# Performance work log

Hardware: AMD Instinct MI355X
Metric: run time of the kernel (lower is better)

The kernel has to match this reference:

```python
import jax, jax.numpy as jnp
import numpy as np

B = 512      # batch
T = 128      # decoder horizon -> T-1 = 127 steps
DNH = 128    # decoder_num_hidden
ENC = 2 * DNH   # encoder_num_hidden (required by attn concat: 3*ENC == 6*DNH)
H = 2 * DNH     # LSTM hidden size


def setup_inputs() -> dict:
    key = jax.random.key(0)
    ks = jax.random.split(key, 10)
    def w(k, shape, scale=0.05):
        return jax.random.normal(k, shape, jnp.float32) * scale
    return {
        "X_encoded": jax.random.normal(ks[0], (B, T - 1, ENC), jnp.float32),
        "y_prev":    jax.random.normal(ks[1], (B, T - 1), jnp.float32),
        # attn_layer: Linear(6*DNH -> DNH) then Linear(DNH -> 1)
        "W_attn1": w(ks[2], (DNH, 6 * DNH)), "b_attn1": jnp.zeros((DNH,), jnp.float32),
        "W_attn2": w(ks[3], (1, DNH)),       "b_attn2": jnp.zeros((1,), jnp.float32),
        # fc: Linear(2*DNH+1 -> 1)
        "W_fc": w(ks[4], (1, 2 * DNH + 1)),  "b_fc": jnp.zeros((1,), jnp.float32),
        # single-layer LSTM, input_size=1, hidden=H, PyTorch gate order (i,f,g,o)
        "W_ih": w(ks[5], (4 * H, 1)), "W_hh": w(ks[6], (4 * H, H)),
        "b_ih": jnp.zeros((4 * H,), jnp.float32), "b_hh": jnp.zeros((4 * H,), jnp.float32),
        # fc_final: Linear(4*DNH -> 1)
        "W_final": w(ks[7], (1, 4 * DNH)), "b_final": jnp.zeros((1,), jnp.float32),
    }


def reference(X_encoded, y_prev, W_attn1, b_attn1, W_attn2, b_attn2,
              W_fc, b_fc, W_ih, W_hh, b_ih, b_hh, W_final, b_final):
    Bz, Tm1, E = X_encoded.shape
    Hh = W_hh.shape[1]
    d0 = jnp.zeros((Bz, Hh), X_encoded.dtype)
    c0 = jnp.zeros((Bz, Hh), X_encoded.dtype)

    def step(carry, y_t):
        d, c = carry                                   # (B, H) each
        state = jnp.concatenate([d, c], axis=-1)[:, None, :]        # (B,1,2H)
        x = jnp.concatenate(
            [jnp.broadcast_to(state, (Bz, Tm1, 2 * Hh)), X_encoded], axis=-1)  # (B,T-1,6*DNH)
        a = x @ W_attn1.T + b_attn1                    # (B,T-1,DNH)
        score = (a @ W_attn2.T + b_attn2)[..., 0]      # (B,T-1)
        beta = jax.nn.softmax(score, axis=1)
        context = jnp.einsum('bt,bte->be', beta, X_encoded)          # (B,E)
        y = jnp.concatenate([context, y_t[:, None]], axis=-1)        # (B,E+1)
        y_tilde = y @ W_fc.T + b_fc                    # (B,1)
        gates = y_tilde @ W_ih.T + b_ih + d @ W_hh.T + b_hh          # (B,4H)
        i, f, g, o = jnp.split(gates, 4, axis=-1)
        i, f, o = jax.nn.sigmoid(i), jax.nn.sigmoid(f), jax.nn.sigmoid(o)
        g = jnp.tanh(g)
        c_new = f * c + i * g
        d_new = o * jnp.tanh(c_new)
        return (d_new, c_new), context

    (dT, _), contexts = jax.lax.scan(step, (d0, c0), y_prev.T)
    y_pred = jnp.concatenate([dT, contexts[-1]], axis=-1) @ W_final.T + b_final  # (B,1)
    return y_pred
```

## Files before the change

kernel.cpp:

```cpp
#include <hip/hip_runtime.h>
#include <stdint.h>

typedef __attribute__((ext_vector_type(8))) short short8;
typedef __attribute__((ext_vector_type(8))) unsigned short ushort8_t;
typedef __attribute__((ext_vector_type(4))) float floatx4;

#define T1 127
#define ENC 256
#define HD 256

#define WHI_OFF   0u
#define WLO_OFF   524288u
#define D0_OFF    1048576u
#define D1_OFF    1572864u
#define WEFF_OFF  2097152u
#define YT_OFF    2099200u
#define CTX_OFF   2361344u
#define DT_OFF    2885632u

__device__ __forceinline__ void split_bf16(float x, unsigned& hi, unsigned& lo) {
    unsigned u = __float_as_uint(x);
    hi = u >> 16;
    float hf = __uint_as_float(hi << 16);
    float r = x - hf;
    unsigned ur = __float_as_uint(r);
    lo = (ur + 0x7fffu + ((ur >> 16) & 1u)) >> 16;
}

__device__ __forceinline__ float sigm_f(float x) { return 1.f / (1.f + __expf(-x)); }
__device__ __forceinline__ float tanh_f(float x) {
    x = fminf(9.f, fmaxf(-9.f, x));
    float e = __expf(2.f * x);
    return (e - 1.f) / (e + 1.f);
}

__global__ __launch_bounds__(256) void k_prep(const float* __restrict__ W1,
                                              const float* __restrict__ W2,
                                              const float* __restrict__ W_hh,
                                              char* __restrict__ ws) {
    const int tid = threadIdx.x, bid = blockIdx.x;
    ushort* Whi = (ushort*)(ws + WHI_OFF);
    ushort* Wlo = (ushort*)(ws + WLO_OFF);
    {
        const int i4 = bid * 256 + tid;
        float4 v = ((const float4*)W_hh)[i4];
        float vv[4] = {v.x, v.y, v.z, v.w};
        unsigned h[4], l[4];
        #pragma unroll
        for (int j = 0; j < 4; ++j) split_bf16(vv[j], h[j], l[j]);
        *(ushort4*)(Whi + i4 * 4) = make_ushort4((ushort)h[0], (ushort)h[1], (ushort)h[2], (ushort)h[3]);
        *(ushort4*)(Wlo + i4 * 4) = make_ushort4((ushort)l[0], (ushort)l[1], (ushort)l[2], (ushort)l[3]);
    }
    {
        const int idx = bid * 256 + tid;
        if (idx < 32768) ((uint4*)(ws + D0_OFF))[idx] = make_uint4(0, 0, 0, 0);
    }
    if (bid == 0) {
        float acc = 0.f;
        for (int j = 0; j < 128; ++j)
            acc = fmaf(W2[j], W1[j * 768 + 512 + tid], acc);
        ((float*)(ws + WEFF_OFF))[tid] = acc;
    }
}

__global__ __launch_bounds__(256) void k_attn(const float* __restrict__ X,
                                              const float* __restrict__ y_prev,
                                              const float* __restrict__ W_fc,
                                              const float* __restrict__ b_fc,
                                              char* __restrict__ ws) {
    __shared__ float s_lds[128];
    __shared__ float beta[128];
    __shared__ float red[256];
    const int b = blockIdx.x, tid = threadIdx.x;
    const int w = tid >> 6, lane = tid & 63;
    const float* Xb = X + (size_t)b * T1 * ENC;
    const float* weff = (const float*)(ws + WEFF_OFF);
    const float4 w4 = ((const float4*)weff)[lane];
    for (int i = 0; i < 32; ++i) {
        int t = w * 32 + i;
        if (t >= T1) break;
        float4 x4 = ((const float4*)(Xb + t * ENC))[lane];
        float a = x4.x * w4.x + x4.y * w4.y + x4.z * w4.z + x4.w * w4.w;
        for (int m = 32; m >= 1; m >>= 1) a += __shfl_xor(a, m, 64);
        if (lane == 0) s_lds[t] = a;
    }
    __syncthreads();
    if (w == 0) {
        float v0 = s_lds[lane];
        float v1 = (lane + 64 < T1) ? s_lds[lane + 64] : -1e30f;
        float mx = fmaxf(v0, v1);
        for (int m = 32; m >= 1; m >>= 1) mx = fmaxf(mx, __shfl_xor(mx, m, 64));
        float e0 = __expf(v0 - mx);
        float e1 = (lane + 64 < T1) ? __expf(v1 - mx) : 0.f;
        float s = e0 + e1;
        for (int m = 32; m >= 1; m >>= 1) s += __shfl_xor(s, m, 64);
        float inv = 1.f / s;
        beta[lane] = e0 * inv;
        if (lane + 64 < T1) beta[lane + 64] = e1 * inv;
    }
    __syncthreads();
    float acc = 0.f;
    for (int t = 0; t < T1; ++t) acc = fmaf(beta[t], Xb[t * ENC + tid], acc);
    ((float*)(ws + CTX_OFF))[b * ENC + tid] = acc;
    red[tid] = acc * W_fc[tid];
    __syncthreads();
    for (int s = 128; s >= 1; s >>= 1) { if (tid < s) red[tid] += red[tid + s]; __syncthreads(); }
    const float u = red[0] + b_fc[0];
    const float wy = W_fc[256];
    if (tid < T1)
        ((float*)(ws + YT_OFF))[b * 128 + tid] = u + wy * y_prev[b * T1 + tid];
}

__global__ __launch_bounds__(256, 1) void k_lstm(const float* __restrict__ W_ih,
                                                 const float* __restrict__ b_ih,
                                                 const float* __restrict__ b_hh,
                                                 char* __restrict__ ws) {
    __shared__ __align__(16) ushort ldh[16 * 264];
    __shared__ __align__(16) ushort ldl[16 * 264];
    __shared__ float gbuf[16 * 132];

    const int tid = threadIdx.x, bid = blockIdx.x;
    const int gi = bid >> 3, hj = bid & 7;
    const int w = tid >> 6, lane = tid & 63;
    const int n16 = lane & 15, q = lane >> 4;

    const ushort* Whi = (const ushort*)(ws + WHI_OFF);
    const ushort* Wlo = (const ushort*)(ws + WLO_OFF);
    unsigned long long* Dbuf0 = (unsigned long long*)(ws + D0_OFF);
    unsigned long long* Dbuf1 = (unsigned long long*)(ws + D1_OFF);
    const float* yt = (const float*)(ws + YT_OFF);
    float* dT = (float*)(ws + DT_OFF);

    short8 bfh[2][8], bfl[2][8];
    #pragma unroll
    for (int j = 0; j < 2; ++j) {
        const int r = (2 * w + j) * 16 + n16;
        const int hloc = r >> 2, g = r & 3;
        const int R = g * 256 + hj * 32 + hloc;
        #pragma unroll
        for (int kt = 0; kt < 8; ++kt) {
            bfh[j][kt] = *(const short8*)(Whi + R * 256 + kt * 32 + q * 8);
            bfl[j][kt] = *(const short8*)(Wlo + R * 256 + kt * 32 + q * 8);
        }
    }

    const int b_loc = tid & 15, hpair = tid >> 4;
    const int hloc0 = hpair * 2;
    const int bg = gi * 16 + b_loc;
    float wihr[2][4], bihr[2][4];
    #pragma unroll
    for (int jj = 0; jj < 2; ++jj)
        #pragma unroll
        for (int g = 0; g < 4; ++g) {
            const int row = g * HD + hj * 32 + hloc0 + jj;
            wihr[jj][g] = W_ih[row];
            bihr[jj][g] = b_ih[row] + b_hh[row];
        }
    float cc0 = 0.f, cc1 = 0.f;

    const int pb = tid >> 4, hp8 = tid & 15;
    const bool own = ((hp8 >> 1) == hj);
    const size_t pbase = (size_t)(gi * 16 + pb) * 128 + hp8 * 8;

    {
        ushort8_t z = {0, 0, 0, 0, 0, 0, 0, 0};
        *(ushort8_t*)(ldh + pb * 264 + hp8 * 16)     = z;
        *(ushort8_t*)(ldh + pb * 264 + hp8 * 16 + 8) = z;
        *(ushort8_t*)(ldl + pb * 264 + hp8 * 16)     = z;
        *(ushort8_t*)(ldl + pb * 264 + hp8 * 16 + 8) = z;
    }

    for (int t = 1; t <= T1; ++t) {
        const float ytv = yt[bg * 128 + (t - 1)];
        if (!own) {
            unsigned long long* Dsrc = ((t - 1) & 1) ? Dbuf1 : Dbuf0;
            const unsigned e = (unsigned)(t - 1) & 3u;
            unsigned long long wv[8];
            #pragma unroll
            for (int i = 0; i < 8; ++i)
                wv[i] = __hip_atomic_load(&Dsrc[pbase + i], __ATOMIC_RELAXED,
                                          __HIP_MEMORY_SCOPE_AGENT);
            unsigned stale = 0xFFu;
            for (;;) {
                unsigned ns = 0;
                #pragma unroll
                for (int i = 0; i < 8; ++i)
                    if (stale & (1u << i)) {
                        unsigned ep = (unsigned)(wv[i] & 1ull) |
                                      (((unsigned)(wv[i] >> 32) & 1u) << 1);
                        if (ep != e) ns |= 1u << i;
                    }
                if (!ns) break;
                __builtin_amdgcn_s_sleep(1);
                #pragma unroll
                for (int i = 0; i < 8; ++i)
                    if (ns & (1u << i))
                        wv[i] = __hip_atomic_load(&Dsrc[pbase + i], __ATOMIC_RELAXED,
                                                  __HIP_MEMORY_SCOPE_AGENT);
                stale = ns;
            }
            ushort hv[16], lv[16];
            #pragma unroll
            for (int i = 0; i < 8; ++i) {
                hv[2 * i]     = (ushort)((wv[i] >> 16) & 0xFFFFull);
                hv[2 * i + 1] = (ushort)(wv[i] >> 48);
                lv[2 * i]     = (ushort)(wv[i] & 0xFFFEull);
                lv[2 * i + 1] = (ushort)((wv[i] >> 32) & 0xFFFEull);
            }
            ushort8_t H0, L0;
            #pragma unroll
            for (int i = 0; i < 8; ++i) { H0[i] = hv[i]; L0[i] = lv[i]; }
            ushort8_t H1, L1;
            #pragma unroll
            for (int i = 0; i < 8; ++i) { H1[i] = hv[8 + i]; L1[i] = lv[8 + i]; }
            *(ushort8_t*)(ldh + pb * 264 + hp8 * 16)     = H0;
            *(ushort8_t*)(ldh + pb * 264 + hp8 * 16 + 8) = H1;
            *(ushort8_t*)(ldl + pb * 264 + hp8 * 16)     = L0;
            *(ushort8_t*)(ldl + pb * 264 + hp8 * 16 + 8) = L1;
        }
        __syncthreads();
        floatx4 acc0 = {0.f, 0.f, 0.f, 0.f}, acc1 = {0.f, 0.f, 0.f, 0.f};
        #pragma unroll
        for (int kt = 0; kt < 8; ++kt) {
            short8 ah = *(const short8*)(ldh + n16 * 264 + kt * 32 + q * 8);
            short8 al = *(const short8*)(ldl + n16 * 264 + kt * 32 + q * 8);
            acc0 = __builtin_amdgcn_mfma_f32_16x16x32_bf16(ah, bfh[0][kt], acc0, 0, 0, 0);
            acc0 = __builtin_amdgcn_mfma_f32_16x16x32_bf16(al, bfh[0][kt], acc0, 0, 0, 0);
            acc0 = __builtin_amdgcn_mfma_f32_16x16x32_bf16(ah, bfl[0][kt], acc0, 0, 0, 0);
            acc1 = __builtin_amdgcn_mfma_f32_16x16x32_bf16(ah, bfh[1][kt], acc1, 0, 0, 0);
            acc1 = __builtin_amdgcn_mfma_f32_16x16x32_bf16(al, bfh[1][kt], acc1, 0, 0, 0);
            acc1 = __builtin_amdgcn_mfma_f32_16x16x32_bf16(ah, bfl[1][kt], acc1, 0, 0, 0);
        }
        #pragma unroll
        for (int reg = 0; reg < 4; ++reg) {
            gbuf[(q * 4 + reg) * 132 + (2 * w) * 16 + n16]     = acc0[reg];
            gbuf[(q * 4 + reg) * 132 + (2 * w + 1) * 16 + n16] = acc1[reg];
        }
        __syncthreads();
        float dnew[2];
        #pragma unroll
        for (int jj = 0; jj < 2; ++jj) {
            const int base = b_loc * 132 + (hloc0 + jj) * 4;
            float pi = gbuf[base + 0] + ytv * wihr[jj][0] + bihr[jj][0];
            float pf = gbuf[base + 1] + ytv * wihr[jj][1] + bihr[jj][1];
            float pg = gbuf[base + 2] + ytv * wihr[jj][2] + bihr[jj][2];
            float po = gbuf[base + 3] + ytv * wihr[jj][3] + bihr[jj][3];
            float ig = sigm_f(pi), fg = sigm_f(pf), og = sigm_f(po);
            float gg = tanh_f(pg);
            float& c = jj ? cc1 : cc0;
            c = fg * c + ig * gg;
            dnew[jj] = og * tanh_f(c);
        }
        if (t < T1) {
            const unsigned e = (unsigned)t & 3u;
            unsigned h0, l0, h1, l1;
            split_bf16(dnew[0], h0, l0);
            split_bf16(dnew[1], h1, l1);
            l0 = (l0 & 0xFFFEu) | (e & 1u);
            l1 = (l1 & 0xFFFEu) | ((e >> 1) & 1u);
            *(ushort2*)(ldh + b_loc * 264 + hj * 32 + hloc0) =
                make_ushort2((ushort)h0, (ushort)h1);
            *(ushort2*)(ldl + b_loc * 264 + hj * 32 + hloc0) =
                make_ushort2((ushort)(l0 & 0xFFFEu), (ushort)(l1 & 0xFFFEu));
            unsigned long long wv = ((unsigned long long)h1 << 48) |
                                    ((unsigned long long)l1 << 32) |
                                    ((unsigned long long)h0 << 16) |
                                    (unsigned long long)l0;
            unsigned long long* Ddst = (t & 1) ? Dbuf1 : Dbuf0;
            __hip_atomic_store(&Ddst[(size_t)bg * 128 + hj * 16 + hpair], wv,
                               __ATOMIC_RELAXED, __HIP_MEMORY_SCOPE_AGENT);
        } else {
            *(float2*)(dT + bg * 256 + hj * 32 + hloc0) = make_float2(dnew[0], dnew[1]);
        }
    }
}

__global__ __launch_bounds__(256) void k_final(const float* __restrict__ W_final,
                                               const float* __restrict__ b_final,
                                               float* __restrict__ out,
                                               char* __restrict__ ws) {
    __shared__ float red[256];
    const int b = blockIdx.x, tid = threadIdx.x;
    const float* dT = (const float*)(ws + DT_OFF);
    const float* ctx = (const float*)(ws + CTX_OFF);
    float v = W_final[tid] * dT[b * 256 + tid] + W_final[256 + tid] * ctx[b * 256 + tid];
    red[tid] = v;
    __syncthreads();
    for (int s = 128; s >= 1; s >>= 1) { if (tid < s) red[tid] += red[tid + s]; __syncthreads(); }
    if (tid == 0) out[b] = red[0] + b_final[0];
}

extern "C" void kernel_launch(void* const* d_in, const int* in_sizes, int n_in,
                              void* d_out, int out_size, void* d_ws, size_t ws_size,
                              hipStream_t stream) {
    const float* X      = (const float*)d_in[0];
    const float* y_prev = (const float*)d_in[1];
    const float* W1     = (const float*)d_in[2];
    const float* W2     = (const float*)d_in[4];
    const float* W_fc   = (const float*)d_in[6];
    const float* b_fc   = (const float*)d_in[7];
    const float* W_ih   = (const float*)d_in[8];
    const float* W_hh   = (const float*)d_in[9];
    const float* b_ih   = (const float*)d_in[10];
    const float* b_hh   = (const float*)d_in[11];
    const float* W_fin  = (const float*)d_in[12];
    const float* b_fin  = (const float*)d_in[13];
    char* ws = (char*)d_ws;

    hipLaunchKernelGGL(k_prep,  dim3(256), dim3(256), 0, stream, W1, W2, W_hh, ws);
    hipLaunchKernelGGL(k_attn,  dim3(512), dim3(256), 0, stream, X, y_prev, W_fc, b_fc, ws);
    hipLaunchKernelGGL(k_lstm,  dim3(256), dim3(256), 0, stream, W_ih, b_ih, b_hh, ws);
    hipLaunchKernelGGL(k_final, dim3(512), dim3(256), 0, stream, W_fin, b_fin, (float*)d_out, ws);
}
```

Measured before the change: 655.2 us.

## Remap LSTM blocks to XCD-local groups and poll with vectorized sc0 loads

Block IDs are remapped so the eight hidden-slice blocks of one batch group land on the same XCD under round-robin dispatch, letting cross-block state exchange stay in a shared L2. The per-step handoff poll is replaced by four wide dwordx4 loads with the sc0 cache bit plus a bounded retry, falling back to the original per-word agent-scope atomic polling if it times out. Each publish now issues a plain non-atomic global store before the existing atomic store. The intent is to cut cross-XCD coherence latency on the serial 127-step chain. The cost is a reliance on the undocumented dispatch-to-XCD mapping and on a weaker cache coherence scope, plus one redundant store per step.

```diff
diff --git a/kernel.cpp b/kernel.cpp
--- a/kernel.cpp
+++ b/kernel.cpp
@@ -32,6 +32,18 @@
     x = fminf(9.f, fmaxf(-9.f, x));
     float e = __expf(2.f * x);
     return (e - 1.f) / (e + 1.f);
+}
+
+__device__ __forceinline__ void load64_sc0(const unsigned long long* p,
+                                           uint4& a, uint4& b, uint4& c, uint4& d) {
+    asm volatile("global_load_dwordx4 %0, %4, off sc0\n\t"
+                 "global_load_dwordx4 %1, %4, off offset:16 sc0\n\t"
+                 "global_load_dwordx4 %2, %4, off offset:32 sc0\n\t"
+                 "global_load_dwordx4 %3, %4, off offset:48 sc0\n\t"
+                 "s_waitcnt vmcnt(0)"
+                 : "=v"(a), "=v"(b), "=v"(c), "=v"(d)
+                 : "v"((unsigned long long)p)
+                 : "memory");
 }
 
 __global__ __launch_bounds__(256) void k_prep(const float* __restrict__ W1,
@@ -120,7 +132,8 @@
     __shared__ float gbuf[16 * 132];
 
     const int tid = threadIdx.x, bid = blockIdx.x;
-    const int gi = bid >> 3, hj = bid & 7;
+    const int gi = (bid & 7) * 4 + (bid >> 6);
+    const int hj = (bid >> 3) & 7;
     const int w = tid >> 6, lane = tid & 63;
     const int n16 = lane & 15, q = lane >> 4;
 
@@ -161,6 +174,7 @@
     const int pb = tid >> 4, hp8 = tid & 15;
     const bool own = ((hp8 >> 1) == hj);
     const size_t pbase = (size_t)(gi * 16 + pb) * 128 + hp8 * 8;
+    bool fast = true;
 
     {
         ushort8_t z = {0, 0, 0, 0, 0, 0, 0, 0};
@@ -175,44 +189,69 @@
         if (!own) {
             unsigned long long* Dsrc = ((t - 1) & 1) ? Dbuf1 : Dbuf0;
             const unsigned e = (unsigned)(t - 1) & 3u;
-            unsigned long long wv[8];
-            #pragma unroll
-            for (int i = 0; i < 8; ++i)
-                wv[i] = __hip_atomic_load(&Dsrc[pbase + i], __ATOMIC_RELAXED,
-                                          __HIP_MEMORY_SCOPE_AGENT);
-            unsigned stale = 0xFFu;
-            for (;;) {
-                unsigned ns = 0;
+            unsigned lo[8], hi[8];
+            bool got = false;
+            if (fast) {
+                for (int rr = 0; rr < 24; ++rr) {
+                    uint4 A, B, C, D;
+                    load64_sc0(&Dsrc[pbase], A, B, C, D);
+                    lo[0] = A.x; hi[0] = A.y; lo[1] = A.z; hi[1] = A.w;
+                    lo[2] = B.x; hi[2] = B.y; lo[3] = B.z; hi[3] = B.w;
+                    lo[4] = C.x; hi[4] = C.y; lo[5] = C.z; hi[5] = C.w;
+                    lo[6] = D.x; hi[6] = D.y; lo[7] = D.z; hi[7] = D.w;
+                    bool ok = true;
+                    #pragma unroll
+                    for (int i = 0; i < 8; ++i) {
+                        unsigned ep = (lo[i] & 1u) | ((hi[i] & 1u) << 1);
+                        ok &= (ep == e);
+                    }
+                    if (ok) { got = true; break; }
+                    __builtin_amdgcn_s_sleep(1);
+                }
+                if (!got) fast = false;
+            }
+            if (!got) {
+                unsigned long long wv[8];
                 #pragma unroll
                 for (int i = 0; i < 8; ++i)
-                    if (stale & (1u << i)) {
-                        unsigned ep = (unsigned)(wv[i] & 1ull) |
-                                      (((unsigned)(wv[i] >> 32) & 1u) << 1);
-                        if (ep != e) ns |= 1u << i;
-                    }
-                if (!ns) break;
-                __builtin_amdgcn_s_sleep(1);
+                    wv[i] = __hip_atomic_load(&Dsrc[pbase + i], __ATOMIC_RELAXED,
+                                              __HIP_MEMORY_SCOPE_AGENT);
+                unsigned stale = 0xFFu;
+                for (;;) {
+                    unsigned ns = 0;
+                    #pragma unroll
+                    for (int i = 0; i < 8; ++i)
+                        if (stale & (1u << i)) {
+                            unsigned ep = (unsigned)(wv[i] & 1ull) |
+                                          (((unsigned)(wv[i] >> 32) & 1u) << 1);
+                            if (ep != e) ns |= 1u << i;
+                        }
+                    if (!ns) break;
+                    __builtin_amdgcn_s_sleep(1);
+                    #pragma unroll
+                    for (int i = 0; i < 8; ++i)
+                        if (ns & (1u << i))
+                            wv[i] = __hip_atomic_load(&Dsrc[pbase + i], __ATOMIC_RELAXED,
+                                                      __HIP_MEMORY_SCOPE_AGENT);
+                    stale = ns;
+                }
                 #pragma unroll
-                for (int i = 0; i < 8; ++i)
-                    if (ns & (1u << i))
-                        wv[i] = __hip_atomic_load(&Dsrc[pbase + i], __ATOMIC_RELAXED,
-                                                  __HIP_MEMORY_SCOPE_AGENT);
-                stale = ns;
+                for (int i = 0; i < 8; ++i) {
+                    lo[i] = (unsigned)wv[i];
+                    hi[i] = (unsigned)(wv[i] >> 32);
+                }
             }
             ushort hv[16], lv[16];
             #pragma unroll
             for (int i = 0; i < 8; ++i) {
-                hv[2 * i]     = (ushort)((wv[i] >> 16) & 0xFFFFull);
-                hv[2 * i + 1] = (ushort)(wv[i] >> 48);
-                lv[2 * i]     = (ushort)(wv[i] & 0xFFFEull);
-                lv[2 * i + 1] = (ushort)((wv[i] >> 32) & 0xFFFEull);
+                hv[2 * i]     = (ushort)(lo[i] >> 16);
+                hv[2 * i + 1] = (ushort)(hi[i] >> 16);
+                lv[2 * i]     = (ushort)(lo[i] & 0xFFFEu);
+                lv[2 * i + 1] = (ushort)(hi[i] & 0xFFFEu);
             }
-            ushort8_t H0, L0;
+            ushort8_t H0, L0, H1, L1;
             #pragma unroll
-            for (int i = 0; i < 8; ++i) { H0[i] = hv[i]; L0[i] = lv[i]; }
-            ushort8_t H1, L1;
-            #pragma unroll
-            for (int i = 0; i < 8; ++i) { H1[i] = hv[8 + i]; L1[i] = lv[8 + i]; }
+            for (int i = 0; i < 8; ++i) { H0[i] = hv[i]; L0[i] = lv[i]; H1[i] = hv[8 + i]; L1[i] = lv[8 + i]; }
             *(ushort8_t*)(ldh + pb * 264 + hp8 * 16)     = H0;
             *(ushort8_t*)(ldh + pb * 264 + hp8 * 16 + 8) = H1;
             *(ushort8_t*)(ldl + pb * 264 + hp8 * 16)     = L0;
@@ -267,8 +306,10 @@
                                     ((unsigned long long)h0 << 16) |
                                     (unsigned long long)l0;
             unsigned long long* Ddst = (t & 1) ? Dbuf1 : Dbuf0;
-            __hip_atomic_store(&Ddst[(size_t)bg * 128 + hj * 16 + hpair], wv,
-                               __ATOMIC_RELAXED, __HIP_MEMORY_SCOPE_AGENT);
+            unsigned long long* dstp = &Ddst[(size_t)bg * 128 + hj * 16 + hpair];
+            asm volatile("global_store_dwordx2 %0, %1, off"
+                         :: "v"((unsigned long long)dstp), "v"(wv) : "memory");
+            __hip_atomic_store(dstp, wv, __ATOMIC_RELAXED, __HIP_MEMORY_SCOPE_AGENT);
         } else {
             *(float2*)(dT + bg * 256 + hj * 32 + hloc0) = make_float2(dnew[0], dnew[1]);
         }
```

Measured after the change: 1.194 ms. 82.2% more time.

## Process two batch groups per LSTM block, interleaving their recurrent steps

Applied to the files above, without the earlier changes.

Each LSTM block now handles two 16-row batch groups instead of one, halving the grid to 128 blocks. Within each timestep it processes the groups one after the other, so one group's cross-block exchange wait can overlap with work on the other, and the register-resident W_hh fragments are reused across both groups. The spin-wait also skips s_sleep for the first two polling rounds to cut wake-up latency. The cost is twice the serial work per block per step and half as many active CUs, so the latency-bound recurrence may lengthen.

```diff
diff --git a/kernel.cpp b/kernel.cpp
--- a/kernel.cpp
+++ b/kernel.cpp
@@ -115,12 +115,12 @@
                                                  const float* __restrict__ b_ih,
                                                  const float* __restrict__ b_hh,
                                                  char* __restrict__ ws) {
-    __shared__ __align__(16) ushort ldh[16 * 264];
-    __shared__ __align__(16) ushort ldl[16 * 264];
+    __shared__ __align__(16) ushort ldh[2][4224];
+    __shared__ __align__(16) ushort ldl[2][4224];
     __shared__ float gbuf[16 * 132];
 
-    const int tid = threadIdx.x, bid = blockIdx.x;
-    const int gi = bid >> 3, hj = bid & 7;
+    const int tid = threadIdx.x, bk = blockIdx.x;
+    const int hj = bk & 7, pi = bk >> 3;
     const int w = tid >> 6, lane = tid & 63;
     const int n16 = lane & 15, q = lane >> 4;
 
@@ -146,7 +146,7 @@
 
     const int b_loc = tid & 15, hpair = tid >> 4;
     const int hloc0 = hpair * 2;
-    const int bg = gi * 16 + b_loc;
+    const int bgs[2] = { (2 * pi) * 16 + b_loc, (2 * pi + 1) * 16 + b_loc };
     float wihr[2][4], bihr[2][4];
     #pragma unroll
     for (int jj = 0; jj < 2; ++jj)
@@ -156,121 +156,129 @@
             wihr[jj][g] = W_ih[row];
             bihr[jj][g] = b_ih[row] + b_hh[row];
         }
-    float cc0 = 0.f, cc1 = 0.f;
+    float cc[2][2] = {{0.f, 0.f}, {0.f, 0.f}};
 
     const int pb = tid >> 4, hp8 = tid & 15;
     const bool own = ((hp8 >> 1) == hj);
-    const size_t pbase = (size_t)(gi * 16 + pb) * 128 + hp8 * 8;
+    const size_t pbases[2] = {
+        ((size_t)((2 * pi) * 16 + pb)) * 128 + hp8 * 8,
+        ((size_t)((2 * pi + 1) * 16 + pb)) * 128 + hp8 * 8
+    };
 
     {
         ushort8_t z = {0, 0, 0, 0, 0, 0, 0, 0};
-        *(ushort8_t*)(ldh + pb * 264 + hp8 * 16)     = z;
-        *(ushort8_t*)(ldh + pb * 264 + hp8 * 16 + 8) = z;
-        *(ushort8_t*)(ldl + pb * 264 + hp8 * 16)     = z;
-        *(ushort8_t*)(ldl + pb * 264 + hp8 * 16 + 8) = z;
+        #pragma unroll
+        for (int s = 0; s < 2; ++s) {
+            *(ushort8_t*)(&ldh[s][pb * 264 + hp8 * 16])     = z;
+            *(ushort8_t*)(&ldh[s][pb * 264 + hp8 * 16 + 8]) = z;
+            *(ushort8_t*)(&ldl[s][pb * 264 + hp8 * 16])     = z;
+            *(ushort8_t*)(&ldl[s][pb * 264 + hp8 * 16 + 8]) = z;
+        }
     }
 
     for (int t = 1; t <= T1; ++t) {
-        const float ytv = yt[bg * 128 + (t - 1)];
-        if (!own) {
-            unsigned long long* Dsrc = ((t - 1) & 1) ? Dbuf1 : Dbuf0;
-            const unsigned e = (unsigned)(t - 1) & 3u;
-            unsigned long long wv[8];
-            #pragma unroll
-            for (int i = 0; i < 8; ++i)
-                wv[i] = __hip_atomic_load(&Dsrc[pbase + i], __ATOMIC_RELAXED,
-                                          __HIP_MEMORY_SCOPE_AGENT);
-            unsigned stale = 0xFFu;
-            for (;;) {
-                unsigned ns = 0;
+        #pragma unroll
+        for (int s = 0; s < 2; ++s) {
+            const int bg = bgs[s];
+            const float ytv = yt[bg * 128 + (t - 1)];
+            if (!own) {
+                unsigned long long* Dsrc = ((t - 1) & 1) ? Dbuf1 : Dbuf0;
+                const unsigned e = (unsigned)(t - 1) & 3u;
+                const size_t pbase = pbases[s];
+                unsigned long long wv[8];
                 #pragma unroll
                 for (int i = 0; i < 8; ++i)
-                    if (stale & (1u << i)) {
-                        unsigned ep = (unsigned)(wv[i] & 1ull) |
-                                      (((unsigned)(wv[i] >> 32) & 1u) << 1);
-                        if (ep != e) ns |= 1u << i;
-                    }
-                if (!ns) break;
-                __builtin_amdgcn_s_sleep(1);
+                    wv[i] = __hip_atomic_load(&Dsrc[pbase + i], __ATOMIC_RELAXED,
+                                              __HIP_MEMORY_SCOPE_AGENT);
+                unsigned stale = 0xFFu;
+                for (int round = 0; ; ++round) {
+                    unsigned ns = 0;
+                    #pragma unroll
+                    for (int i = 0; i < 8; ++i)
+                        if (stale & (1u << i)) {
+                            unsigned ep = (unsigned)(wv[i] & 1ull) |
+                                          (((unsigned)(wv[i] >> 32) & 1u) << 1);
+                            if (ep != e) ns |= 1u << i;
+                        }
+                    if (!ns) break;
+                    if (round >= 2) __builtin_amdgcn_s_sleep(1);
+                    #pragma unroll
+                    for (int i = 0; i < 8; ++i)
+                        if (ns & (1u << i))
+                            wv[i] = __hip_atomic_load(&Dsrc[pbase + i], __ATOMIC_RELAXED,
+                                                      __HIP_MEMORY_SCOPE_AGENT);
+                    stale = ns;
+                }
+                ushort hv[16], lv[16];
                 #pragma unroll
-                for (int i = 0; i < 8; ++i)
-                    if (ns & (1u << i))
-                        wv[i] = __hip_atomic_load(&Dsrc[pbase + i], __ATOMIC_RELAXED,
-                                                  __HIP_MEMORY_SCOPE_AGENT);
-                stale = ns;
-            }
-            ushort hv[16], lv[16];
+                for (int i = 0; i < 8; ++i) {
+                    hv[2 * i]     = (ushort)((wv[i] >> 16) & 0xFFFFull);
+                    hv[2 * i + 1] = (ushort)(wv[i] >> 48);
+                    lv[2 * i]     = (ushort)(wv[i] & 0xFFFEull);
+                    lv[2 * i + 1] = (ushort)((wv[i] >> 32) & 0xFFFEull);
+                }
+                ushort8_t H0, L0, H1, L1;
+                #pragma unroll
+                for (int i = 0; i < 8; ++i) { H0[i] = hv[i]; L0[i] = lv[i]; H1[i] = hv[8 + i]; L1[i] = lv[8 + i]; }
+                *(ushort8_t*)(&ldh[s][pb * 264 + hp8 * 16])     = H0;
+                *(ushort8_t*)(&ldh[s][pb * 264 + hp8 * 16 + 8]) = H1;
+                *(ushort8_t*)(&ldl[s][pb * 264 + hp8 * 16])     = L0;
+                *(ushort8_t*)(&ldl[s][pb * 264 + hp8 * 16 + 8]) = L1;
+            }
+            __syncthreads();
+            floatx4 acc0 = {0.f, 0.f, 0.f, 0.f}, acc1 = {0.f, 0.f, 0.f, 0.f};
             #pragma unroll
-            for (int i = 0; i < 8; ++i) {
-                hv[2 * i]     = (ushort)((wv[i] >> 16) & 0xFFFFull);
-                hv[2 * i + 1] = (ushort)(wv[i] >> 48);
-                lv[2 * i]     = (ushort)(wv[i] & 0xFFFEull);
-                lv[2 * i + 1] = (ushort)((wv[i] >> 32) & 0xFFFEull);
-            }
-            ushort8_t H0, L0;
+            for (int kt = 0; kt < 8; ++kt) {
+                short8 ah = *(const short8*)(&ldh[s][n16 * 264 + kt * 32 + q * 8]);
+                short8 al = *(const short8*)(&ldl[s][n16 * 264 + kt * 32 + q * 8]);
+                acc0 = __builtin_amdgcn_mfma_f32_16x16x32_bf16(ah, bfh[0][kt], acc0, 0, 0, 0);
+                acc0 = __builtin_amdgcn_mfma_f32_16x16x32_bf16(al, bfh[0][kt], acc0, 0, 0, 0);
+                acc0 = __builtin_amdgcn_mfma_f32_16x16x32_bf16(ah, bfl[0][kt], acc0, 0, 0, 0);
+                acc1 = __builtin_amdgcn_mfma_f32_16x16x32_bf16(ah, bfh[1][kt], acc1, 0, 0, 0);
+                acc1 = __builtin_amdgcn_mfma_f32_16x16x32_bf16(al, bfh[1][kt], acc1, 0, 0, 0);
+                acc1 = __builtin_amdgcn_mfma_f32_16x16x32_bf16(ah, bfl[1][kt], acc1, 0, 0, 0);
+            }
             #pragma unroll
-            for (int i = 0; i < 8; ++i) { H0[i] = hv[i]; L0[i] = lv[i]; }
-            ushort8_t H1, L1;
+            for (int reg = 0; reg < 4; ++reg) {
+                gbuf[(q * 4 + reg) * 132 + (2 * w) * 16 + n16]     = acc0[reg];
+                gbuf[(q * 4 + reg) * 132 + (2 * w + 1) * 16 + n16] = acc1[reg];
+            }
+            __syncthreads();
+            float dnew[2];
             #pragma unroll
-            for (int i = 0; i < 8; ++i) { H1[i] = hv[8 + i]; L1[i] = lv[8 + i]; }
-            *(ushort8_t*)(ldh + pb * 264 + hp8 * 16)     = H0;
-            *(ushort8_t*)(ldh + pb * 264 + hp8 * 16 + 8) = H1;
-            *(ushort8_t*)(ldl + pb * 264 + hp8 * 16)     = L0;
-            *(ushort8_t*)(ldl + pb * 264 + hp8 * 16 + 8) = L1;
-        }
-        __syncthreads();
-        floatx4 acc0 = {0.f, 0.f, 0.f, 0.f}, acc1 = {0.f, 0.f, 0.f, 0.f};
-        #pragma unroll
-        for (int kt = 0; kt < 8; ++kt) {
-            short8 ah = *(const short8*)(ldh + n16 * 264 + kt * 32 + q * 8);
-            short8 al = *(const short8*)(ldl + n16 * 264 + kt * 32 + q * 8);
-            acc0 = __builtin_amdgcn_mfma_f32_16x16x32_bf16(ah, bfh[0][kt], acc0, 0, 0, 0);
-            acc0 = __builtin_amdgcn_mfma_f32_16x16x32_bf16(al, bfh[0][kt], acc0, 0, 0, 0);
-            acc0 = __builtin_amdgcn_mfma_f32_16x16x32_bf16(ah, bfl[0][kt], acc0, 0, 0, 0);
-            acc1 = __builtin_amdgcn_mfma_f32_16x16x32_bf16(ah, bfh[1][kt], acc1, 0, 0, 0);
-            acc1 = __builtin_amdgcn_mfma_f32_16x16x32_bf16(al, bfh[1][kt], acc1, 0, 0, 0);
-            acc1 = __builtin_amdgcn_mfma_f32_16x16x32_bf16(ah, bfl[1][kt], acc1, 0, 0, 0);
-        }
-        #pragma unroll
-        for (int reg = 0; reg < 4; ++reg) {
-            gbuf[(q * 4 + reg) * 132 + (2 * w) * 16 + n16]     = acc0[reg];
-            gbuf[(q * 4 + reg) * 132 + (2 * w + 1) * 16 + n16] = acc1[reg];
-        }
-        __syncthreads();
-        float dnew[2];
-        #pragma unroll
-        for (int jj = 0; jj < 2; ++jj) {
-            const int base = b_loc * 132 + (hloc0 + jj) * 4;
-            float pi = gbuf[base + 0] + ytv * wihr[jj][0] + bihr[jj][0];
-            float pf = gbuf[base + 1] + ytv * wihr[jj][1] + bihr[jj][1];
-            float pg = gbuf[base + 2] + ytv * wihr[jj][2] + bihr[jj][2];
-            float po = gbuf[base + 3] + ytv * wihr[jj][3] + bihr[jj][3];
-            float ig = sigm_f(pi), fg = sigm_f(pf), og = sigm_f(po);
-            float gg = tanh_f(pg);
-            float& c = jj ? cc1 : cc0;
-            c = fg * c + ig * gg;
-            dnew[jj] = og * tanh_f(c);
-        }
-        if (t < T1) {
-            const unsigned e = (unsigned)t & 3u;
-            unsigned h0, l0, h1, l1;
-            split_bf16(dnew[0], h0, l0);
-            split_bf16(dnew[1], h1, l1);
-            l0 = (l0 & 0xFFFEu) | (e & 1u);
-            l1 = (l1 & 0xFFFEu) | ((e >> 1) & 1u);
-            *(ushort2*)(ldh + b_loc * 264 + hj * 32 + hloc0) =
-                make_ushort2((ushort)h0, (ushort)h1);
-            *(ushort2*)(ldl + b_loc * 264 + hj * 32 + hloc0) =
-                make_ushort2((ushort)(l0 & 0xFFFEu), (ushort)(l1 & 0xFFFEu));
-            unsigned long long wv = ((unsigned long long)h1 << 48) |
-                                    ((unsigned long long)l1 << 32) |
-                                    ((unsigned long long)h0 << 16) |
-                                    (unsigned long long)l0;
-            unsigned long long* Ddst = (t & 1) ? Dbuf1 : Dbuf0;
-            __hip_atomic_store(&Ddst[(size_t)bg * 128 + hj * 16 + hpair], wv,
-                               __ATOMIC_RELAXED, __HIP_MEMORY_SCOPE_AGENT);
-        } else {
-            *(float2*)(dT + bg * 256 + hj * 32 + hloc0) = make_float2(dnew[0], dnew[1]);
+            for (int jj = 0; jj < 2; ++jj) {
+                const int base = b_loc * 132 + (hloc0 + jj) * 4;
+                float pi_ = gbuf[base + 0] + ytv * wihr[jj][0] + bihr[jj][0];
+                float pf  = gbuf[base + 1] + ytv * wihr[jj][1] + bihr[jj][1];
+                float pg  = gbuf[base + 2] + ytv * wihr[jj][2] + bihr[jj][2];
+                float po  = gbuf[base + 3] + ytv * wihr[jj][3] + bihr[jj][3];
+                float ig = sigm_f(pi_), fg = sigm_f(pf), og = sigm_f(po);
+                float gg = tanh_f(pg);
+                float& c = cc[s][jj];
+                c = fg * c + ig * gg;
+                dnew[jj] = og * tanh_f(c);
+            }
+            if (t < T1) {
+                const unsigned e = (unsigned)t & 3u;
+                unsigned h0, l0, h1, l1;
+                split_bf16(dnew[0], h0, l0);
+                split_bf16(dnew[1], h1, l1);
+                l0 = (l0 & 0xFFFEu) | (e & 1u);
+                l1 = (l1 & 0xFFFEu) | ((e >> 1) & 1u);
+                *(ushort2*)(&ldh[s][b_loc * 264 + hj * 32 + hloc0]) =
+                    make_ushort2((ushort)h0, (ushort)h1);
+                *(ushort2*)(&ldl[s][b_loc * 264 + hj * 32 + hloc0]) =
+                    make_ushort2((ushort)(l0 & 0xFFFEu), (ushort)(l1 & 0xFFFEu));
+                unsigned long long wv = ((unsigned long long)h1 << 48) |
+                                        ((unsigned long long)l1 << 32) |
+                                        ((unsigned long long)h0 << 16) |
+                                        (unsigned long long)l0;
+                unsigned long long* Ddst = (t & 1) ? Dbuf1 : Dbuf0;
+                __hip_atomic_store(&Ddst[(size_t)bg * 128 + hj * 16 + hpair], wv,
+                                   __ATOMIC_RELAXED, __HIP_MEMORY_SCOPE_AGENT);
+            } else {
+                *(float2*)(dT + bg * 256 + hj * 32 + hloc0) = make_float2(dnew[0], dnew[1]);
+            }
         }
     }
 }
@@ -309,6 +317,6 @@
 
     hipLaunchKernelGGL(k_prep,  dim3(256), dim3(256), 0, stream, W1, W2, W_hh, ws);
     hipLaunchKernelGGL(k_attn,  dim3(512), dim3(256), 0, stream, X, y_prev, W_fc, b_fc, ws);
-    hipLaunchKernelGGL(k_lstm,  dim3(256), dim3(256), 0, stream, W_ih, b_ih, b_hh, ws);
+    hipLaunchKernelGGL(k_lstm,  dim3(128), dim3(256), 0, stream, W_ih, b_ih, b_hh, ws);
     hipLaunchKernelGGL(k_final, dim3(512), dim3(256), 0, stream, W_fin, b_fin, (float*)d_out, ws);
 }
```

After: 831.1 us. 1.27x slower.
